# Kernel tuning notes

Measured on AMD Instinct MI355X. Metric: run time of the kernel, lower is better.

## Reference

```python
import jax, jax.numpy as jnp
import numpy as np

# region/recall params from layer config
NUM_CLASSES = 20
NUM_ANCHORS = 5
ANCHORS = jnp.array([[1.3221, 1.73145], [3.19275, 4.00944], [5.05587, 8.09892],
                     [9.47112, 4.84053], [11.2364, 10.0071]], dtype=jnp.float32)
CONF_THRESH = 0.5
NMS_THRESH = 0.45
IOU_THRESH = 0.5
EPS = 1e-6


def setup_inputs() -> dict:
    key = jax.random.key(0)
    k1, k2 = jax.random.split(key)
    output = jax.random.normal(k1, (8, NUM_ANCHORS * (5 + NUM_CLASSES), 19, 19), dtype=jnp.float32)
    target = jax.random.uniform(k2, (8, 250), dtype=jnp.float32)  # [B, 50*5] rows: cls,cx,cy,w,h
    return {"output": output, "target": target}


def decode_region_boxes(output):
    """get_region_boxes: anchor decode. output [B, A*(5+C), H, W] -> boxes [B, A*H*W, 4] cxcywh (normalized), det_conf [B, A*H*W]."""
    B, _, H, W = output.shape
    o = output.reshape(B, NUM_ANCHORS, 5 + NUM_CLASSES, H, W)
    gx = jnp.arange(W, dtype=output.dtype)
    gy = jnp.arange(H, dtype=output.dtype)
    cx = (jax.nn.sigmoid(o[:, :, 0]) + gx[None, None, None, :]) / W
    cy = (jax.nn.sigmoid(o[:, :, 1]) + gy[None, None, :, None]) / H
    bw = jnp.exp(o[:, :, 2]) * (ANCHORS[:, 0] / W)[None, :, None, None]
    bh = jnp.exp(o[:, :, 3]) * (ANCHORS[:, 1] / H)[None, :, None, None]
    det_conf = jax.nn.sigmoid(o[:, :, 4])
    boxes = jnp.stack([cx, cy, bw, bh], axis=-1).reshape(B, -1, 4)
    return boxes, det_conf.reshape(B, -1)


def pairwise_iou(a, b):
    """bbox_iou(x1y1x2y2=False) for all pairs. a [..., Na, 4], b [..., Nb, 4] cxcywh -> [..., Na, Nb]."""
    ax1 = (a[..., 0] - a[..., 2] * 0.5)[..., :, None]
    ax2 = (a[..., 0] + a[..., 2] * 0.5)[..., :, None]
    ay1 = (a[..., 1] - a[..., 3] * 0.5)[..., :, None]
    ay2 = (a[..., 1] + a[..., 3] * 0.5)[..., :, None]
    bx1 = (b[..., 0] - b[..., 2] * 0.5)[..., None, :]
    bx2 = (b[..., 0] + b[..., 2] * 0.5)[..., None, :]
    by1 = (b[..., 1] - b[..., 3] * 0.5)[..., None, :]
    by2 = (b[..., 1] + b[..., 3] * 0.5)[..., None, :]
    uw = jnp.maximum(ax2, bx2) - jnp.minimum(ax1, bx1)
    uh = jnp.maximum(ay2, by2) - jnp.minimum(ay1, by1)
    aw = a[..., 2][..., :, None]; ah = a[..., 3][..., :, None]
    bw = b[..., 2][..., None, :]; bh = b[..., 3][..., None, :]
    cw = aw + bw - uw
    ch = ah + bh - uh
    carea = jnp.where((cw > 0) & (ch > 0), cw * ch, 0.0)
    uarea = aw * ah + bw * bh - carea
    return carea / uarea


def greedy_nms_keep(iou_mat, valid):
    """Sequential greedy NMS over conf-sorted boxes using precomputed IoU. iou_mat [N,N], valid [N] bool."""
    N = valid.shape[0]
    idx = jnp.arange(N)
    def body(i, keep):
        sup = keep[i] & (iou_mat[i] > NMS_THRESH) & (idx > i)
        return keep & (~sup)
    return jax.lax.fori_loop(0, N, body, valid)


def reference(output, target):
    B = output.shape[0]
    boxes, det = decode_region_boxes(output)              # [B,N,4], [B,N]
    # sort by det_conf descending (nms sort order)
    order = jnp.argsort(-det, axis=1)
    boxes = jnp.take_along_axis(boxes, order[..., None], axis=1)
    det = jnp.take_along_axis(det, order, axis=1)
    valid = det > CONF_THRESH                             # boxes that enter nms (conf filter in get_region_boxes)
    iou_mat = pairwise_iou(boxes, boxes)                  # [B,N,N]
    keep = jax.vmap(greedy_nms_keep)(iou_mat, valid)      # [B,N]
    proposals = jnp.sum(keep)
    # ground truth: [B,T,5] rows [cls,cx,cy,w,h]; num_gts = boxes until first cx==0
    truths = target.reshape(B, -1, 5)
    gt_valid = jnp.cumprod((truths[..., 1] != 0).astype(jnp.int32), axis=1).astype(bool)  # [B,T]
    total = jnp.sum(gt_valid)
    iou_gt = pairwise_iou(truths[..., 1:5], boxes)        # [B,T,N]
    best_iou = jnp.max(jnp.where(keep[:, None, :], iou_gt, 0.0), axis=-1)  # [B,T]
    correct = jnp.sum(gt_valid & (best_iou > IOU_THRESH))
    total_f = total.astype(jnp.float32)
    prop_f = proposals.astype(jnp.float32)
    corr_f = correct.astype(jnp.float32)
    precision = corr_f / (prop_f + EPS)
    recall = corr_f / (total_f + EPS)
    fscore = 2.0 * precision * recall / (precision + recall + EPS)
    return jnp.stack([total_f, prop_f, corr_f, precision, recall, fscore])
```

## Files before the change

kernel.cpp:

```cpp
#include <hip/hip_runtime.h>

namespace {
constexpr int NA    = 5;
constexpr int NCELL = 361;
constexpr int NBOX  = 1805;
constexpr int NBOXP = 1856;
constexpr int NT1   = 1024;
constexpr int TMAX  = 50;
constexpr float CONF_T = 0.5f;
constexpr float NMS_T  = 0.45f;
constexpr float IOU_T  = 0.5f;
constexpr int NW     = 29;
constexpr int NWMAX  = 32;
constexpr int SOA_STRIDE = NBOXP;
constexpr int SOA_ARR    = 8 * SOA_STRIDE;
constexpr int TRIW = 64 * (NW * (NW + 1) / 2);
constexpr size_t WS_COUNT = 0;
constexpr size_t WS_M     = 64;
constexpr size_t WS_SOA   = 256;
constexpr size_t WS_SUP   = 360448;
__device__ inline size_t tri_off(int w) { return (size_t)32 * w * (w + 1); }
}

__device__ __constant__ float d_anchw[NA] = {1.3221f, 3.19275f, 5.05587f, 9.47112f, 11.2364f};
__device__ __constant__ float d_anchh[NA] = {1.73145f, 4.00944f, 8.09892f, 4.84053f, 10.0071f};

__device__ inline unsigned long long rdlane64(unsigned long long v, int l) {
    unsigned lo = (unsigned)__builtin_amdgcn_readlane((int)(unsigned)(v & 0xffffffffull), l);
    unsigned hi = (unsigned)__builtin_amdgcn_readlane((int)(unsigned)(v >> 32), l);
    return ((unsigned long long)hi << 32) | lo;
}
__device__ inline void barrier_lgkm() {
    __asm__ volatile("" ::: "memory");
    __builtin_amdgcn_s_waitcnt(0xC07F);
    __builtin_amdgcn_s_barrier();
    __asm__ volatile("" ::: "memory");
}

__global__ __launch_bounds__(NT1, 1) void k_decode_sort(
    const float* __restrict__ net, float* __restrict__ soa,
    int* __restrict__ Marr, int* __restrict__ counters)
{
    __shared__ unsigned long long skey[2048];
    __shared__ float4 sbox[NBOX];
    __shared__ int sCnt;
    const int b = blockIdx.x, tid = threadIdx.x, lane = tid & 63;
    const float* op = net + (size_t)b * (NA * 25 * NCELL);
    if (tid == 0) sCnt = 0;
    if (b == 0 && tid < 4) counters[tid] = 0;
    __syncthreads();

    for (int n = tid; n < NBOX; n += NT1) {
        int a = n / NCELL;
        int r = n - a * NCELL;
        int y = r / 19;
        int x = r - y * 19;
        int base = a * 25 * NCELL + r;
        float t0 = op[base];
        float t1 = op[base + 1 * NCELL];
        float t2 = op[base + 2 * NCELL];
        float t3 = op[base + 3 * NCELL];
        float t4 = op[base + 4 * NCELL];
        float cx = (1.0f / (1.0f + expf(-t0)) + (float)x) / 19.0f;
        float cy = (1.0f / (1.0f + expf(-t1)) + (float)y) / 19.0f;
        float bw = expf(t2) * (d_anchw[a] / 19.0f);
        float bh = expf(t3) * (d_anchh[a] / 19.0f);
        float det = 1.0f / (1.0f + expf(-t4));
        sbox[n] = make_float4(cx, cy, bw, bh);
        bool valid = det > CONF_T;
        unsigned long long bm = __ballot(valid);
        int base0 = 0;
        if (lane == 0 && bm) base0 = atomicAdd(&sCnt, __popcll(bm));
        base0 = __shfl(base0, 0, 64);
        if (valid) {
            int pos = base0 + __popcll(bm & ((1ull << lane) - 1ull));
            skey[pos] = ((unsigned long long)(~__float_as_uint(det)) << 32) | (unsigned)n;
        }
    }
    __syncthreads();
    const int M = sCnt;
    int S = 64; while (S < M) S <<= 1;
    for (int n = M + tid; n < S; n += NT1) skey[n] = ~0ull;
    __syncthreads();

    unsigned long long v[8];
    const int nt8 = S >> 3;
    const int base8 = tid << 3;
    auto cas = [&](int xx, int yy, bool up) {
        unsigned long long a = v[xx], c = v[yy];
        if ((a > c) == up) { v[xx] = c; v[yy] = a; }
    };
    if (tid < nt8) {
        #pragma unroll
        for (int p = 0; p < 8; ++p) v[p] = skey[base8 + p];
        cas(0,1,true); cas(2,3,false); cas(4,5,true); cas(6,7,false);
        cas(0,2,true); cas(1,3,true); cas(4,6,false); cas(5,7,false);
        cas(0,1,true); cas(2,3,true); cas(4,5,false); cas(6,7,false);
        bool u8 = ((base8 & 8) == 0);
        cas(0,4,u8); cas(1,5,u8); cas(2,6,u8); cas(3,7,u8);
        cas(0,2,u8); cas(1,3,u8); cas(4,6,u8); cas(5,7,u8);
        cas(0,1,u8); cas(2,3,u8); cas(4,5,u8); cas(6,7,u8);
        #pragma unroll
        for (int p = 0; p < 8; ++p) skey[base8 + p] = v[p];
    }
    __syncthreads();
    for (unsigned k = 16; k <= (unsigned)S; k <<= 1) {
        for (unsigned j = k >> 1; j >= 8; j >>= 1) {
            for (unsigned m = tid; m < (unsigned)(S >> 1); m += NT1) {
                unsigned i = ((m & ~(j - 1)) << 1) | (m & (j - 1));
                unsigned p = i | j;
                bool up = ((i & k) == 0);
                unsigned long long a = skey[i], c2 = skey[p];
                if ((a > c2) == up) { skey[i] = c2; skey[p] = a; }
            }
            __syncthreads();
        }
        if (tid < nt8) {
            #pragma unroll
            for (int p = 0; p < 8; ++p) v[p] = skey[base8 + p];
            bool up = ((base8 & k) == 0);
            cas(0,4,up); cas(1,5,up); cas(2,6,up); cas(3,7,up);
            cas(0,2,up); cas(1,3,up); cas(4,6,up); cas(5,7,up);
            cas(0,1,up); cas(2,3,up); cas(4,5,up); cas(6,7,up);
            #pragma unroll
            for (int p = 0; p < 8; ++p) skey[base8 + p] = v[p];
        }
        __syncthreads();
    }

    float* X1 = soa + 0 * SOA_ARR + b * SOA_STRIDE;
    float* Y1 = soa + 1 * SOA_ARR + b * SOA_STRIDE;
    float* X2 = soa + 2 * SOA_ARR + b * SOA_STRIDE;
    float* Y2 = soa + 3 * SOA_ARR + b * SOA_STRIDE;
    float* Wd = soa + 4 * SOA_ARR + b * SOA_STRIDE;
    float* Hd = soa + 5 * SOA_ARR + b * SOA_STRIDE;
    const int mceil = (M + 63) & ~63;
    for (int p = tid; p < mceil; p += NT1) {
        float4 bx = make_float4(0.f, 0.f, 0.f, 0.f);
        if (p < M) bx = sbox[(unsigned)(skey[p] & 0xffffffffull)];
        X1[p] = bx.x - 0.5f * bx.z;
        Y1[p] = bx.y - 0.5f * bx.w;
        X2[p] = bx.x + 0.5f * bx.z;
        Y2[p] = bx.y + 0.5f * bx.w;
        Wd[p] = bx.z;
        Hd[p] = bx.w;
    }
    if (tid == 0) Marr[b] = M;
}

__global__ __launch_bounds__(256) void k_iou_maskT(
    const float* __restrict__ soa, const int* __restrict__ Marr,
    unsigned long long* __restrict__ supT)
{
    const int blk  = blockIdx.x;
    const int b    = blk & 7;
    const int g    = blk >> 3;
    const int wv   = threadIdx.x >> 6;
    const int lane = threadIdx.x & 63;
    const int M = Marr[b];
    const int i0 = g * 16 + wv * 4;
    if (i0 >= M) return;
    const float* X1 = soa + 0 * SOA_ARR + b * SOA_STRIDE;
    const float* Y1 = soa + 1 * SOA_ARR + b * SOA_STRIDE;
    const float* X2 = soa + 2 * SOA_ARR + b * SOA_STRIDE;
    const float* Y2 = soa + 3 * SOA_ARR + b * SOA_STRIDE;
    const float* Wd = soa + 4 * SOA_ARR + b * SOA_STRIDE;
    const float* Hd = soa + 5 * SOA_ARR + b * SOA_STRIDE;
    const int nch = (M + 63) >> 6;
    const int w0  = i0 >> 6;

    float ax1[4], ay1[4], ax2[4], ay2[4], aw[4], ah[4], aarea[4];
    #pragma unroll
    for (int r = 0; r < 4; ++r) {
        int ir = i0 + r; if (ir >= M) ir = M - 1;
        ax1[r] = X1[ir]; ay1[r] = Y1[ir];
        ax2[r] = X2[ir]; ay2[r] = Y2[ir];
        aw[r]  = Wd[ir]; ah[r]  = Hd[ir];
        aarea[r] = aw[r] * ah[r];
    }
    unsigned long long myw0 = 0, myw1 = 0, myw2 = 0, myw3 = 0;
    for (int w = w0; w < nch; ++w) {
        int j = (w << 6) + lane;
        float bx1 = X1[j], by1 = Y1[j];
        float bx2 = X2[j], by2 = Y2[j];
        float bw  = Wd[j], bh  = Hd[j];
        float barea = bw * bh;
        bool jok = (j < M);
        #pragma unroll
        for (int r = 0; r < 4; ++r) {
            bool pred = false;
            if (jok && j > i0 + r) {
                float uw = fmaxf(ax2[r], bx2) - fminf(ax1[r], bx1);
                float uh = fmaxf(ay2[r], by2) - fminf(ay1[r], by1);
                float cw = aw[r] + bw - uw;
                float ch = ah[r] + bh - uh;
                if (cw > 0.0f && ch > 0.0f) {
                    float ca = cw * ch;
                    float ua = aarea[r] + barea - ca;
                    pred = ca > NMS_T * ua;
                }
            }
            unsigned long long m = __ballot(pred);
            if (w == lane) {
                if      (r == 0) myw0 = m;
                else if (r == 1) myw1 = m;
                else if (r == 2) myw2 = m;
                else             myw3 = m;
            }
        }
    }
    if (lane >= w0 && lane < nch) {
        unsigned long long* dst = supT + (size_t)b * TRIW + tri_off(lane);
        dst[i0] = myw0;
        if (i0 + 1 < M) dst[i0 + 1] = myw1;
        if (i0 + 2 < M) dst[i0 + 2] = myw2;
        if (i0 + 3 < M) dst[i0 + 3] = myw3;
    }
}

__global__ __launch_bounds__(1024, 1) void k_sweep(
    const float* __restrict__ soa, const float* __restrict__ tgt,
    const int* __restrict__ Marr, const unsigned long long* __restrict__ supT,
    int* __restrict__ counters, float* __restrict__ out)
{
    __shared__ float X1s[NBOXP], Y1s[NBOXP], X2s[NBOXP], Y2s[NBOXP];
    __shared__ float Wss[NBOXP], Hss[NBOXP];
    __shared__ unsigned rmwU[2 * NWMAX];
    __shared__ unsigned long long keepw[NWMAX];
    __shared__ int sNV, sCorr, sProp;
    const int b = blockIdx.x, tid = threadIdx.x;
    const int wv = tid >> 6, lane = tid & 63;
    const int M = Marr[b];
    const int nwa = (M + 63) >> 6;
    const unsigned long long* sb = supT + (size_t)b * TRIW;

    if (tid < 2 * NWMAX) rmwU[tid] = 0u;
    if (tid < NWMAX) keepw[tid] = 0ull;
    if (tid == 0) { sCorr = 0; sProp = 0; }

    {
        int mceil = (M + 63) & ~63;
        const float* X1 = soa + 0 * SOA_ARR + b * SOA_STRIDE;
        const float* Y1 = soa + 1 * SOA_ARR + b * SOA_STRIDE;
        const float* X2 = soa + 2 * SOA_ARR + b * SOA_STRIDE;
        const float* Y2 = soa + 3 * SOA_ARR + b * SOA_STRIDE;
        const float* Wd = soa + 4 * SOA_ARR + b * SOA_STRIDE;
        const float* Hd = soa + 5 * SOA_ARR + b * SOA_STRIDE;
        for (int p = tid; p < mceil; p += 1024) {
            X1s[p] = X1[p]; Y1s[p] = Y1[p];
            X2s[p] = X2[p]; Y2s[p] = Y2[p];
            Wss[p] = Wd[p]; Hss[p] = Hd[p];
        }
    }
    if (wv == 2) {
        float cxv = (lane < TMAX) ? tgt[b * 250 + lane * 5 + 1] : 0.0f;
        unsigned long long bm = __ballot(cxv != 0.0f);
        unsigned long long inv = (~bm) & ((1ull << TMAX) - 1ull);
        if (lane == 0) sNV = inv ? (__ffsll((long long)inv) - 1) : TMAX;
    }

    const int w1 = (wv >= 1) ? wv : -1;
    const int w2 = (wv >= 1 && wv + 15 <= 28) ? (wv + 15) : -1;
    unsigned long long cur1 = 0, cur2 = 0, diag = 0;
    if (wv == 0 && nwa > 0) diag = sb[tri_off(0) + lane];
    if (w1 >= 1 && w1 < nwa) cur1 = sb[tri_off(w1) + lane];
    if (w2 >= 1 && w2 < nwa) cur2 = sb[tri_off(w2) + lane];
    __syncthreads();

    for (int t = 0; t < nwa; ++t) {
        if (wv == 0) {
            unsigned long long cur =
                ((unsigned long long)rmwU[2 * t + 1] << 32) | rmwU[2 * t];
            int rem = M - (t << 6);
            unsigned long long vm = (rem >= 64) ? ~0ull : ((1ull << rem) - 1ull);
            unsigned long long live = vm & ~cur;
            while (live) {
                int i = __ffsll((long long)live) - 1;
                unsigned long long w64 = rdlane64(diag, i);
                cur |= w64;
                live &= ~w64;
                live &= ~(1ull << i);
            }
            unsigned long long kp = vm & ~cur;
            if (lane == 0) keepw[t] = kp;
            int tn = t + 1;
            if (tn < nwa) diag = sb[tri_off(tn) + (tn << 6) + lane];
        }
        barrier_lgkm();
        {
            unsigned long long kmt = keepw[t];
            bool kept = (kmt >> lane) & 1ull;
            if (w1 > t && w1 < nwa && kept) {
                unsigned lo = (unsigned)cur1, hi = (unsigned)(cur1 >> 32);
                if (lo) atomicOr(&rmwU[2 * w1], lo);
                if (hi) atomicOr(&rmwU[2 * w1 + 1], hi);
            }
            if (w2 > t && w2 < nwa && kept) {
                unsigned lo = (unsigned)cur2, hi = (unsigned)(cur2 >> 32);
                if (lo) atomicOr(&rmwU[2 * w2], lo);
                if (hi) atomicOr(&rmwU[2 * w2 + 1], hi);
            }
            if (w1 > t + 1 && w1 < nwa) cur1 = sb[tri_off(w1) + ((t + 1) << 6) + lane];
            if (w2 > t + 1 && w2 < nwa) cur2 = sb[tri_off(w2) + ((t + 1) << 6) + lane];
        }
        barrier_lgkm();
    }

    if (wv == 0) {
        unsigned long long kv = (lane < NWMAX) ? keepw[lane] : 0ull;
        int pc = __popcll(kv);
        for (int d = 32; d > 0; d >>= 1) pc += __shfl_down(pc, d, 64);
        if (lane == 0) sProp = pc;
    }

    const int nv = sNV;
    for (int t = wv; t < nv; t += 16) {
        const float* g = tgt + b * 250 + t * 5;
        float gcx = g[1], gcy = g[2], gw = g[3], gh = g[4];
        float gx1 = gcx - 0.5f * gw, gx2 = gcx + 0.5f * gw;
        float gy1 = gcy - 0.5f * gh, gy2 = gcy + 0.5f * gh;
        float garea = gw * gh;
        float best = 0.0f;
        for (int j0 = 0; j0 < M; j0 += 64) {
            unsigned long long kw = keepw[j0 >> 6];
            if (kw == 0ull) continue;
            int j = j0 + lane;
            bool ok = (j < M) && ((kw >> lane) & 1ull);
            int js = (j < NBOXP) ? j : (NBOXP - 1);
            float bw = Wss[js], bh = Hss[js];
            float uw = fmaxf(gx2, X2s[js]) - fminf(gx1, X1s[js]);
            float uh = fmaxf(gy2, Y2s[js]) - fminf(gy1, Y1s[js]);
            float cww = gw + bw - uw, chh = gh + bh - uh;
            float ca = (cww > 0.0f && chh > 0.0f) ? cww * chh : 0.0f;
            float ua = garea + bw * bh - ca;
            float iou = ca / ua;
            best = fmaxf(best, ok ? iou : 0.0f);
        }
        for (int d = 32; d > 0; d >>= 1) best = fmaxf(best, __shfl_down(best, d, 64));
        if (lane == 0 && best > IOU_T) atomicAdd(&sCorr, 1);
    }
    barrier_lgkm();

    if (tid == 0) {
        atomicAdd(counters + 0, sProp);
        atomicAdd(counters + 1, sCorr);
        atomicAdd(counters + 2, sNV);
        __threadfence();
        int done = atomicAdd(counters + 3, 1);
        if (done == 7) {
            float prop  = (float)atomicAdd(counters + 0, 0);
            float corr  = (float)atomicAdd(counters + 1, 0);
            float total = (float)atomicAdd(counters + 2, 0);
            float prec = corr / (prop + 1e-6f);
            float rec  = corr / (total + 1e-6f);
            float fs   = 2.0f * prec * rec / (prec + rec + 1e-6f);
            out[0] = total;
            out[1] = prop;
            out[2] = corr;
            out[3] = prec;
            out[4] = rec;
            out[5] = fs;
        }
    }
}

extern "C" void kernel_launch(void* const* d_in, const int* in_sizes, int n_in,
                              void* d_out, int out_size, void* d_ws, size_t ws_size,
                              hipStream_t stream) {
    const float* net = (const float*)d_in[0];
    const float* tgt = (const float*)d_in[1];
    char* ws = (char*)d_ws;
    int* counters = (int*)(ws + WS_COUNT);
    int* Marr     = (int*)(ws + WS_M);
    float* soa    = (float*)(ws + WS_SOA);
    unsigned long long* supT = (unsigned long long*)(ws + WS_SUP);

    k_decode_sort<<<8, NT1, 0, stream>>>(net, soa, Marr, counters);
    int rowblocks = (NBOX + 15) / 16;
    k_iou_maskT<<<rowblocks * 8, 256, 0, stream>>>(soa, Marr, supT);
    k_sweep<<<8, 1024, 0, stream>>>(soa, tgt, Marr, supT, counters, (float*)d_out);
}
```

Measured before the change: 128.7 us.

## Process two NMS bitmask blocks per round to halve block-wide barriers

Measured after the change: 126.5 us, median of 2. Within noise of the previous version (-1.7%).

```diff
diff --git a/kernel.cpp b/kernel.cpp
--- a/kernel.cpp
+++ b/kernel.cpp
@@ -261,47 +261,109 @@
 
     const int w1 = (wv >= 1) ? wv : -1;
     const int w2 = (wv >= 1 && wv + 15 <= 28) ? (wv + 15) : -1;
-    unsigned long long cur1 = 0, cur2 = 0, diag = 0;
-    if (wv == 0 && nwa > 0) diag = sb[tri_off(0) + lane];
-    if (w1 >= 1 && w1 < nwa) cur1 = sb[tri_off(w1) + lane];
-    if (w2 >= 1 && w2 < nwa) cur2 = sb[tri_off(w2) + lane];
+    unsigned long long dAA = 0, dAB = 0, dBB = 0;
+    unsigned long long curA1 = 0, curB1 = 0, curA2 = 0, curB2 = 0;
+    if (wv == 0 && nwa > 0) {
+        dAA = sb[tri_off(0) + lane];
+        if (nwa > 1) {
+            dAB = sb[tri_off(1) + lane];
+            dBB = sb[tri_off(1) + 64 + lane];
+        }
+    }
+    if (w1 >= 1 && w1 < nwa) {
+        curA1 = sb[tri_off(w1) + lane];
+        curB1 = sb[tri_off(w1) + 64 + lane];
+    }
+    if (w2 >= 1 && w2 < nwa) {
+        curA2 = sb[tri_off(w2) + lane];
+        curB2 = sb[tri_off(w2) + 64 + lane];
+    }
     __syncthreads();
 
-    for (int t = 0; t < nwa; ++t) {
+    const int nr = (nwa + 1) >> 1;
+    for (int r = 0; r < nr; ++r) {
+        const int tA = 2 * r, tB = 2 * r + 1;
         if (wv == 0) {
-            unsigned long long cur =
-                ((unsigned long long)rmwU[2 * t + 1] << 32) | rmwU[2 * t];
-            int rem = M - (t << 6);
-            unsigned long long vm = (rem >= 64) ? ~0ull : ((1ull << rem) - 1ull);
-            unsigned long long live = vm & ~cur;
-            while (live) {
-                int i = __ffsll((long long)live) - 1;
-                unsigned long long w64 = rdlane64(diag, i);
-                cur |= w64;
-                live &= ~w64;
-                live &= ~(1ull << i);
-            }
-            unsigned long long kp = vm & ~cur;
-            if (lane == 0) keepw[t] = kp;
-            int tn = t + 1;
-            if (tn < nwa) diag = sb[tri_off(tn) + (tn << 6) + lane];
+            unsigned long long curA =
+                ((unsigned long long)rmwU[2 * tA + 1] << 32) | rmwU[2 * tA];
+            int remA = M - (tA << 6);
+            unsigned long long vmA = (remA >= 64) ? ~0ull : ((1ull << remA) - 1ull);
+            unsigned long long liveA = vmA & ~curA;
+            unsigned long long nxtB = 0;
+            while (liveA) {
+                int i = __ffsll((long long)liveA) - 1;
+                unsigned long long wA = rdlane64(dAA, i);
+                unsigned long long wB = rdlane64(dAB, i);
+                curA |= wA;
+                nxtB |= wB;
+                liveA &= ~wA;
+                liveA &= ~(1ull << i);
+            }
+            unsigned long long keepA = vmA & ~curA;
+            if (lane == 0) keepw[tA] = keepA;
+            if (tB < nwa) {
+                unsigned long long curB =
+                    (((unsigned long long)rmwU[2 * tB + 1] << 32) | rmwU[2 * tB]) | nxtB;
+                int remB = M - (tB << 6);
+                unsigned long long vmB = (remB >= 64) ? ~0ull : ((1ull << remB) - 1ull);
+                unsigned long long liveB = vmB & ~curB;
+                while (liveB) {
+                    int i = __ffsll((long long)liveB) - 1;
+                    unsigned long long wB = rdlane64(dBB, i);
+                    curB |= wB;
+                    liveB &= ~wB;
+                    liveB &= ~(1ull << i);
+                }
+                if (lane == 0) keepw[tB] = vmB & ~curB;
+            }
+            int nA = tA + 2, nB = tA + 3;
+            if (nA < nwa) {
+                dAA = sb[tri_off(nA) + (nA << 6) + lane];
+                if (nB < nwa) {
+                    dAB = sb[tri_off(nB) + (nA << 6) + lane];
+                    dBB = sb[tri_off(nB) + (nB << 6) + lane];
+                } else { dAB = 0; dBB = 0; }
+            }
         }
         barrier_lgkm();
         {
-            unsigned long long kmt = keepw[t];
-            bool kept = (kmt >> lane) & 1ull;
-            if (w1 > t && w1 < nwa && kept) {
-                unsigned lo = (unsigned)cur1, hi = (unsigned)(cur1 >> 32);
-                if (lo) atomicOr(&rmwU[2 * w1], lo);
-                if (hi) atomicOr(&rmwU[2 * w1 + 1], hi);
-            }
-            if (w2 > t && w2 < nwa && kept) {
-                unsigned lo = (unsigned)cur2, hi = (unsigned)(cur2 >> 32);
-                if (lo) atomicOr(&rmwU[2 * w2], lo);
-                if (hi) atomicOr(&rmwU[2 * w2 + 1], hi);
-            }
-            if (w1 > t + 1 && w1 < nwa) cur1 = sb[tri_off(w1) + ((t + 1) << 6) + lane];
-            if (w2 > t + 1 && w2 < nwa) cur2 = sb[tri_off(w2) + ((t + 1) << 6) + lane];
+            unsigned long long kmtA = keepw[tA];
+            unsigned long long kmtB = (tB < nwa) ? keepw[tB] : 0ull;
+            bool keptA = (kmtA >> lane) & 1ull;
+            bool keptB = (kmtB >> lane) & 1ull;
+            if (w1 > tB && w1 < nwa) {
+                if (keptA) {
+                    unsigned lo = (unsigned)curA1, hi = (unsigned)(curA1 >> 32);
+                    if (lo) atomicOr(&rmwU[2 * w1], lo);
+                    if (hi) atomicOr(&rmwU[2 * w1 + 1], hi);
+                }
+                if (keptB) {
+                    unsigned lo = (unsigned)curB1, hi = (unsigned)(curB1 >> 32);
+                    if (lo) atomicOr(&rmwU[2 * w1], lo);
+                    if (hi) atomicOr(&rmwU[2 * w1 + 1], hi);
+                }
+            }
+            if (w2 > tB && w2 < nwa) {
+                if (keptA) {
+                    unsigned lo = (unsigned)curA2, hi = (unsigned)(curA2 >> 32);
+                    if (lo) atomicOr(&rmwU[2 * w2], lo);
+                    if (hi) atomicOr(&rmwU[2 * w2 + 1], hi);
+                }
+                if (keptB) {
+                    unsigned lo = (unsigned)curB2, hi = (unsigned)(curB2 >> 32);
+                    if (lo) atomicOr(&rmwU[2 * w2], lo);
+                    if (hi) atomicOr(&rmwU[2 * w2 + 1], hi);
+                }
+            }
+            int nA = tA + 2, nB = tA + 3;
+            if (w1 > nB && w1 < nwa) {
+                curA1 = sb[tri_off(w1) + (nA << 6) + lane];
+                curB1 = sb[tri_off(w1) + (nB << 6) + lane];
+            }
+            if (w2 > nB && w2 < nwa) {
+                curA2 = sb[tri_off(w2) + (nA << 6) + lane];
+                curB2 = sb[tri_off(w2) + (nB << 6) + lane];
+            }
         }
         barrier_lgkm();
     }
```

## Block NMS sweep into groups of four words to cut block barriers

Applied to the files above, without the earlier changes.

After: 133.1 us. 1.03x slower.

```diff
diff --git a/kernel.cpp b/kernel.cpp
--- a/kernel.cpp
+++ b/kernel.cpp
@@ -261,47 +261,185 @@
 
     const int w1 = (wv >= 1) ? wv : -1;
     const int w2 = (wv >= 1 && wv + 15 <= 28) ? (wv + 15) : -1;
-    unsigned long long cur1 = 0, cur2 = 0, diag = 0;
-    if (wv == 0 && nwa > 0) diag = sb[tri_off(0) + lane];
-    if (w1 >= 1 && w1 < nwa) cur1 = sb[tri_off(w1) + lane];
-    if (w2 >= 1 && w2 < nwa) cur2 = sb[tri_off(w2) + lane];
+    unsigned long long g00 = 0, g01 = 0, g02 = 0, g03 = 0;
+    unsigned long long g11 = 0, g12 = 0, g13 = 0;
+    unsigned long long g22 = 0, g23 = 0, g33 = 0;
+    unsigned long long c0_1 = 0, c1_1 = 0, c2_1 = 0, c3_1 = 0;
+    unsigned long long c0_2 = 0, c1_2 = 0, c2_2 = 0, c3_2 = 0;
+    if (wv == 0 && nwa > 0) {
+        g00 = sb[tri_off(0) + lane];
+        if (nwa > 1) { g01 = sb[tri_off(1) + lane];
+                       g11 = sb[tri_off(1) + 64 + lane]; }
+        if (nwa > 2) { g02 = sb[tri_off(2) + lane];
+                       g12 = sb[tri_off(2) + 64 + lane];
+                       g22 = sb[tri_off(2) + 128 + lane]; }
+        if (nwa > 3) { g03 = sb[tri_off(3) + lane];
+                       g13 = sb[tri_off(3) + 64 + lane];
+                       g23 = sb[tri_off(3) + 128 + lane];
+                       g33 = sb[tri_off(3) + 192 + lane]; }
+    }
+    if (w1 > 3 && w1 < nwa) {
+        c0_1 = sb[tri_off(w1) + lane];
+        c1_1 = sb[tri_off(w1) + 64 + lane];
+        c2_1 = sb[tri_off(w1) + 128 + lane];
+        c3_1 = sb[tri_off(w1) + 192 + lane];
+    }
+    if (w2 > 3 && w2 < nwa) {
+        c0_2 = sb[tri_off(w2) + lane];
+        c1_2 = sb[tri_off(w2) + 64 + lane];
+        c2_2 = sb[tri_off(w2) + 128 + lane];
+        c3_2 = sb[tri_off(w2) + 192 + lane];
+    }
     __syncthreads();
 
-    for (int t = 0; t < nwa; ++t) {
+    const int nr = (nwa + 3) >> 2;
+    for (int r = 0; r < nr; ++r) {
+        const int t0 = 4 * r, t1 = t0 + 1, t2 = t0 + 2, t3 = t0 + 3;
         if (wv == 0) {
-            unsigned long long cur =
-                ((unsigned long long)rmwU[2 * t + 1] << 32) | rmwU[2 * t];
-            int rem = M - (t << 6);
-            unsigned long long vm = (rem >= 64) ? ~0ull : ((1ull << rem) - 1ull);
-            unsigned long long live = vm & ~cur;
-            while (live) {
-                int i = __ffsll((long long)live) - 1;
-                unsigned long long w64 = rdlane64(diag, i);
-                cur |= w64;
-                live &= ~w64;
-                live &= ~(1ull << i);
-            }
-            unsigned long long kp = vm & ~cur;
-            if (lane == 0) keepw[t] = kp;
-            int tn = t + 1;
-            if (tn < nwa) diag = sb[tri_off(tn) + (tn << 6) + lane];
+            unsigned long long nxt1 = 0, nxt2 = 0, nxt3 = 0;
+            {
+                unsigned long long cur =
+                    ((unsigned long long)rmwU[2 * t0 + 1] << 32) | rmwU[2 * t0];
+                int rem = M - (t0 << 6);
+                unsigned long long vm = (rem >= 64) ? ~0ull : ((1ull << rem) - 1ull);
+                unsigned long long live = vm & ~cur;
+                while (live) {
+                    int i = __ffsll((long long)live) - 1;
+                    unsigned long long w64 = rdlane64(g00, i);
+                    nxt1 |= rdlane64(g01, i);
+                    nxt2 |= rdlane64(g02, i);
+                    nxt3 |= rdlane64(g03, i);
+                    cur |= w64;
+                    live &= ~w64;
+                    live &= ~(1ull << i);
+                }
+                if (lane == 0) keepw[t0] = vm & ~cur;
+            }
+            if (t1 < nwa) {
+                unsigned long long cur =
+                    (((unsigned long long)rmwU[2 * t1 + 1] << 32) | rmwU[2 * t1]) | nxt1;
+                int rem = M - (t1 << 6);
+                unsigned long long vm = (rem >= 64) ? ~0ull : ((1ull << rem) - 1ull);
+                unsigned long long live = vm & ~cur;
+                while (live) {
+                    int i = __ffsll((long long)live) - 1;
+                    unsigned long long w64 = rdlane64(g11, i);
+                    nxt2 |= rdlane64(g12, i);
+                    nxt3 |= rdlane64(g13, i);
+                    cur |= w64;
+                    live &= ~w64;
+                    live &= ~(1ull << i);
+                }
+                if (lane == 0) keepw[t1] = vm & ~cur;
+            }
+            if (t2 < nwa) {
+                unsigned long long cur =
+                    (((unsigned long long)rmwU[2 * t2 + 1] << 32) | rmwU[2 * t2]) | nxt2;
+                int rem = M - (t2 << 6);
+                unsigned long long vm = (rem >= 64) ? ~0ull : ((1ull << rem) - 1ull);
+                unsigned long long live = vm & ~cur;
+                while (live) {
+                    int i = __ffsll((long long)live) - 1;
+                    unsigned long long w64 = rdlane64(g22, i);
+                    nxt3 |= rdlane64(g23, i);
+                    cur |= w64;
+                    live &= ~w64;
+                    live &= ~(1ull << i);
+                }
+                if (lane == 0) keepw[t2] = vm & ~cur;
+            }
+            if (t3 < nwa) {
+                unsigned long long cur =
+                    (((unsigned long long)rmwU[2 * t3 + 1] << 32) | rmwU[2 * t3]) | nxt3;
+                int rem = M - (t3 << 6);
+                unsigned long long vm = (rem >= 64) ? ~0ull : ((1ull << rem) - 1ull);
+                unsigned long long live = vm & ~cur;
+                while (live) {
+                    int i = __ffsll((long long)live) - 1;
+                    unsigned long long w64 = rdlane64(g33, i);
+                    cur |= w64;
+                    live &= ~w64;
+                    live &= ~(1ull << i);
+                }
+                if (lane == 0) keepw[t3] = vm & ~cur;
+            }
+            int n0 = t0 + 4, n1 = t0 + 5, n2 = t0 + 6, n3 = t0 + 7;
+            if (n0 < nwa) {
+                g00 = sb[tri_off(n0) + (n0 << 6) + lane];
+                g01 = (n1 < nwa) ? sb[tri_off(n1) + (n0 << 6) + lane] : 0ull;
+                g11 = (n1 < nwa) ? sb[tri_off(n1) + (n1 << 6) + lane] : 0ull;
+                g02 = (n2 < nwa) ? sb[tri_off(n2) + (n0 << 6) + lane] : 0ull;
+                g12 = (n2 < nwa) ? sb[tri_off(n2) + (n1 << 6) + lane] : 0ull;
+                g22 = (n2 < nwa) ? sb[tri_off(n2) + (n2 << 6) + lane] : 0ull;
+                g03 = (n3 < nwa) ? sb[tri_off(n3) + (n0 << 6) + lane] : 0ull;
+                g13 = (n3 < nwa) ? sb[tri_off(n3) + (n1 << 6) + lane] : 0ull;
+                g23 = (n3 < nwa) ? sb[tri_off(n3) + (n2 << 6) + lane] : 0ull;
+                g33 = (n3 < nwa) ? sb[tri_off(n3) + (n3 << 6) + lane] : 0ull;
+            }
         }
         barrier_lgkm();
         {
-            unsigned long long kmt = keepw[t];
-            bool kept = (kmt >> lane) & 1ull;
-            if (w1 > t && w1 < nwa && kept) {
-                unsigned lo = (unsigned)cur1, hi = (unsigned)(cur1 >> 32);
-                if (lo) atomicOr(&rmwU[2 * w1], lo);
-                if (hi) atomicOr(&rmwU[2 * w1 + 1], hi);
-            }
-            if (w2 > t && w2 < nwa && kept) {
-                unsigned lo = (unsigned)cur2, hi = (unsigned)(cur2 >> 32);
-                if (lo) atomicOr(&rmwU[2 * w2], lo);
-                if (hi) atomicOr(&rmwU[2 * w2 + 1], hi);
-            }
-            if (w1 > t + 1 && w1 < nwa) cur1 = sb[tri_off(w1) + ((t + 1) << 6) + lane];
-            if (w2 > t + 1 && w2 < nwa) cur2 = sb[tri_off(w2) + ((t + 1) << 6) + lane];
+            unsigned long long k0m = keepw[t0];
+            unsigned long long k1m = (t1 < nwa) ? keepw[t1] : 0ull;
+            unsigned long long k2m = (t2 < nwa) ? keepw[t2] : 0ull;
+            unsigned long long k3m = (t3 < nwa) ? keepw[t3] : 0ull;
+            if (w1 > t3 && w1 < nwa) {
+                if ((k0m >> lane) & 1ull) {
+                    unsigned lo = (unsigned)c0_1, hi = (unsigned)(c0_1 >> 32);
+                    if (lo) atomicOr(&rmwU[2 * w1], lo);
+                    if (hi) atomicOr(&rmwU[2 * w1 + 1], hi);
+                }
+                if ((k1m >> lane) & 1ull) {
+                    unsigned lo = (unsigned)c1_1, hi = (unsigned)(c1_1 >> 32);
+                    if (lo) atomicOr(&rmwU[2 * w1], lo);
+                    if (hi) atomicOr(&rmwU[2 * w1 + 1], hi);
+                }
+                if ((k2m >> lane) & 1ull) {
+                    unsigned lo = (unsigned)c2_1, hi = (unsigned)(c2_1 >> 32);
+                    if (lo) atomicOr(&rmwU[2 * w1], lo);
+                    if (hi) atomicOr(&rmwU[2 * w1 + 1], hi);
+                }
+                if ((k3m >> lane) & 1ull) {
+                    unsigned lo = (unsigned)c3_1, hi = (unsigned)(c3_1 >> 32);
+                    if (lo) atomicOr(&rmwU[2 * w1], lo);
+                    if (hi) atomicOr(&rmwU[2 * w1 + 1], hi);
+                }
+            }
+            if (w2 > t3 && w2 < nwa) {
+                if ((k0m >> lane) & 1ull) {
+                    unsigned lo = (unsigned)c0_2, hi = (unsigned)(c0_2 >> 32);
+                    if (lo) atomicOr(&rmwU[2 * w2], lo);
+                    if (hi) atomicOr(&rmwU[2 * w2 + 1], hi);
+                }
+                if ((k1m >> lane) & 1ull) {
+                    unsigned lo = (unsigned)c1_2, hi = (unsigned)(c1_2 >> 32);
+                    if (lo) atomicOr(&rmwU[2 * w2], lo);
+                    if (hi) atomicOr(&rmwU[2 * w2 + 1], hi);
+                }
+                if ((k2m >> lane) & 1ull) {
+                    unsigned lo = (unsigned)c2_2, hi = (unsigned)(c2_2 >> 32);
+                    if (lo) atomicOr(&rmwU[2 * w2], lo);
+                    if (hi) atomicOr(&rmwU[2 * w2 + 1], hi);
+                }
+                if ((k3m >> lane) & 1ull) {
+                    unsigned lo = (unsigned)c3_2, hi = (unsigned)(c3_2 >> 32);
+                    if (lo) atomicOr(&rmwU[2 * w2], lo);
+                    if (hi) atomicOr(&rmwU[2 * w2 + 1], hi);
+                }
+            }
+            int n0 = t0 + 4, n1 = t0 + 5, n2 = t0 + 6, n3 = t0 + 7;
+            if (w1 > n3 && w1 < nwa) {
+                c0_1 = sb[tri_off(w1) + (n0 << 6) + lane];
+                c1_1 = sb[tri_off(w1) + (n1 << 6) + lane];
+                c2_1 = sb[tri_off(w1) + (n2 << 6) + lane];
+                c3_1 = sb[tri_off(w1) + (n3 << 6) + lane];
+            }
+            if (w2 > n3 && w2 < nwa) {
+                c0_2 = sb[tri_off(w2) + (n0 << 6) + lane];
+                c1_2 = sb[tri_off(w2) + (n1 << 6) + lane];
+                c2_2 = sb[tri_off(w2) + (n2 << 6) + lane];
+                c3_2 = sb[tri_off(w2) + (n3 << 6) + lane];
+            }
         }
         barrier_lgkm();
     }
```
